# Kernel optimization log

Measured on AMD Instinct MI355X. Metric: run time of the kernel, lower is better.

## Reference

```python
import jax, jax.numpy as jnp
import numpy as np

K = 3
STRIDE = 1
PAD = 1
GROUPS = 16
EPS = 1e-5


def _conv2d(x, w, b, stride, pad):
    out = jax.lax.conv_general_dilated(
        x, w, (stride, stride), [(pad, pad), (pad, pad)],
        dimension_numbers=("NCHW", "OIHW", "NCHW"))
    return out + b[None, :, None, None]


def setup_inputs() -> dict:
    key = jax.random.key(0)
    ks = jax.random.split(key, 6)
    B, Cin, H, W = 4, 256, 64, 64
    Cout = 256
    x = jax.random.normal(ks[0], (B, Cin, H, W), dtype=jnp.float32)
    # DCNv2 offset/mask-generating conv: 3*K*K = 27 output channels
    w_off = jax.random.normal(ks[1], (3 * K * K, Cin, K, K), dtype=jnp.float32) * 0.01
    b_off = jnp.zeros((3 * K * K,), dtype=jnp.float32)
    # main deformable conv weight/bias
    weight = jax.random.normal(ks[2], (Cout, Cin, K, K), dtype=jnp.float32) * 0.02
    bias = jnp.zeros((Cout,), dtype=jnp.float32)
    # GroupNorm affine params
    gamma = jnp.ones((Cout,), dtype=jnp.float32)
    beta = jnp.zeros((Cout,), dtype=jnp.float32)
    return {"x": x, "w_off": w_off, "b_off": b_off,
            "weight": weight, "bias": bias, "gamma": gamma, "beta": beta}


def reference(x, w_off, b_off, weight, bias, gamma, beta):
    B, Cin, H, W = x.shape
    Cout = weight.shape[0]
    KK = K * K

    # --- offset/mask branch (DCNv2): 18 offsets + 9 sigmoid masks ---
    om = _conv2d(x, w_off, b_off, STRIDE, PAD)          # [B, 27, Ho, Wo]
    Ho, Wo = om.shape[2], om.shape[3]
    off_y, off_x, m = jnp.split(om, 3, axis=1)          # each [B, 9, Ho, Wo]
    mask = jax.nn.sigmoid(m)

    # --- sampling coordinates: base grid + kernel tap + learned offset ---
    kgy = jnp.repeat(jnp.arange(K, dtype=x.dtype), K)   # [9] row of tap
    kgx = jnp.tile(jnp.arange(K, dtype=x.dtype), K)     # [9] col of tap
    base_y = jnp.arange(Ho, dtype=x.dtype) * STRIDE - PAD
    base_x = jnp.arange(Wo, dtype=x.dtype) * STRIDE - PAD
    py = base_y[None, None, :, None] + kgy[None, :, None, None] + off_y  # [B,9,Ho,Wo]
    px = base_x[None, None, None, :] + kgx[None, :, None, None] + off_x  # [B,9,Ho,Wo]

    # --- bilinear sampling with zero padding outside the image ---
    y0 = jnp.floor(py)
    x0 = jnp.floor(px)
    wy1 = py - y0
    wx1 = px - x0

    def gather(img, yy, xx):
        # img [Cin,H,W], yy/xx [9,Ho,Wo] int -> [Cin,9,Ho,Wo]
        return img[:, yy, xx]

    def corner(yi, xi, wy, wx):
        valid = (yi >= 0) & (yi < H) & (xi >= 0) & (xi < W)
        yc = jnp.clip(yi, 0, H - 1).astype(jnp.int32)
        xc = jnp.clip(xi, 0, W - 1).astype(jnp.int32)
        vals = jax.vmap(gather)(x, yc, xc)               # [B,Cin,9,Ho,Wo]
        w_ = (wy * wx * valid.astype(x.dtype))[:, None]   # [B,1,9,Ho,Wo]
        return vals * w_

    sampled = (corner(y0, x0, (1 - wy1), (1 - wx1))
               + corner(y0, x0 + 1, (1 - wy1), wx1)
               + corner(y0 + 1, x0, wy1, (1 - wx1))
               + corner(y0 + 1, x0 + 1, wy1, wx1))       # [B,Cin,9,Ho,Wo]
    sampled = sampled * mask[:, None]                     # modulation

    # --- conv accumulation over taps and input channels ---
    out = jnp.einsum("bckhw,ock->bohw", sampled,
                     weight.reshape(Cout, Cin, KK)) + bias[None, :, None, None]

    # --- GroupNorm(16, Cout) ---
    og = out.reshape(B, GROUPS, Cout // GROUPS, Ho, Wo)
    mu = og.mean(axis=(2, 3, 4), keepdims=True)
    var = og.var(axis=(2, 3, 4), keepdims=True)
    og = (og - mu) * jax.lax.rsqrt(var + EPS)
    out = og.reshape(B, Cout, Ho, Wo) * gamma[None, :, None, None] + beta[None, :, None, None]
    return out
```

## Files before the change

kernel.cpp:

```cpp
#include <hip/hip_runtime.h>
#include <math.h>

#define CIN   256
#define COUT  256
#define H     64
#define W     64
#define HW    4096
#define KK    9
#define KC    2304
#define NOFF  27
#define B_    4
#define EPS   1e-5f
#define OM3S  (B_ * NOFF * HW)

typedef __attribute__((ext_vector_type(4))) float f32x4;
typedef __attribute__((ext_vector_type(8))) short s16x8;

static __device__ __forceinline__ unsigned short f2bf(float f) {
  unsigned u = __builtin_bit_cast(unsigned, f);
  u += 0x7FFF + ((u >> 16) & 1);
  return (unsigned short)(u >> 16);
}
static __device__ __forceinline__ float bflo(unsigned u) {
  return __builtin_bit_cast(float, u << 16);
}
static __device__ __forceinline__ float bfhi(unsigned u) {
  return __builtin_bit_cast(float, u & 0xffff0000u);
}
static __device__ __forceinline__ unsigned packbf(float lo, float hi) {
  unsigned ul = __builtin_bit_cast(unsigned, lo);
  unsigned uh = __builtin_bit_cast(unsigned, hi);
  ul += 0x7FFF + ((ul >> 16) & 1);
  uh += 0x7FFF + ((uh >> 16) & 1);
  return (ul >> 16) | (uh & 0xffff0000u);
}
static __device__ __forceinline__ void gl2lds16(const void* g, void* l) {
  __builtin_amdgcn_global_load_lds(
      (const __attribute__((address_space(1))) unsigned int*)g,
      (__attribute__((address_space(3))) unsigned int*)l, 16, 0, 0);
}

__global__ __launch_bounds__(256) void prep_kernel(
    const float* __restrict__ x, const float* __restrict__ w,
    const float* __restrict__ w_off, unsigned short* __restrict__ xT,
    unsigned short* __restrict__ wBf, unsigned short* __restrict__ wOBf,
    float* __restrict__ gstat) {
  int bi = blockIdx.x;
  int t = threadIdx.x;
  if (bi < 256) {
    __shared__ unsigned short tile[64][272];
    int b = bi >> 6, y = bi & 63;
    const float* src = x + (size_t)b * CIN * HW + y * W;
    for (int r = 0; r < 64; ++r) {
      int idx = r * 256 + t;
      int c = idx >> 6, ww = idx & 63;
      tile[ww][c] = f2bf(src[(size_t)c * HW + ww]);
    }
    __syncthreads();
    unsigned short* dst = xT + ((size_t)(b * 64 + y) * 64) * 256;
    for (int r = 0; r < 8; ++r) {
      int idx = r * 2048 + t * 8;
      int ww = idx >> 8, c = idx & 255;
      *(uint4*)(dst + idx) = *(const uint4*)&tile[ww][c];
    }
  } else if (bi < 544) {
    int pkt = (bi - 256) * 256 + t;
    int lane = pkt & 63;
    int tn = (pkt >> 6) & 15;
    int k2 = pkt >> 10;
    int co = tn * 16 + (lane & 15);
    int kb = k2 * 32 + (lane >> 4) * 8;
    unsigned short v[8];
#pragma unroll
    for (int j = 0; j < 8; ++j) {
      int kk = kb + j;
      int kt = kk >> 8, c = kk & 255;
      v[j] = f2bf(w[(co * 256 + c) * 9 + kt]);
    }
    *(uint4*)&wBf[(size_t)pkt * 8] = *(const uint4*)v;
  } else if (bi < 580) {
    int pkt = (bi - 544) * 256 + t;
    int lane = pkt & 63;
    int tn = (pkt >> 6) & 1;
    int k2 = pkt >> 7;
    int oc = tn * 16 + (lane & 15);
    int kb = k2 * 32 + (lane >> 4) * 8;
    unsigned short v[8];
#pragma unroll
    for (int j = 0; j < 8; ++j) {
      int kk = kb + j;
      int kt = kk >> 8, c = kk & 255;
      v[j] = (oc < NOFF) ? f2bf(w_off[(oc * 256 + c) * 9 + kt]) : (unsigned short)0;
    }
    *(uint4*)&wOBf[(size_t)pkt * 8] = *(const uint4*)v;
  } else {
    if (t < 128) gstat[t] = 0.f;
  }
}

__global__ __launch_bounds__(256) void offconv_mfma_kernel(
    const unsigned short* __restrict__ xT, const unsigned short* __restrict__ wOBf,
    float* __restrict__ om3) {
  int bi = blockIdx.x;
  int ts = bi >> 8;
  int row = bi & 255;
  int b = row >> 6, i = row & 63;
  int t = threadIdx.x, lane = t & 63, wv = t >> 6;
  int lr = lane & 15, lq = lane >> 4;
  int p = wv * 16 + lr;
  const unsigned short* xb = xT + (size_t)b * (HW * 256);
  f32x4 acc[2] = {};

  for (int kc = 0; kc < 3; ++kc) {
    int kt = ts * 3 + kc;
    int ky = kt / 3, kx = kt % 3;
    int yy = i - 1 + ky, xx = p - 1 + kx;
    bool ok = ((unsigned)yy < 64u) && ((unsigned)xx < 64u);
    const unsigned short* ap = xb + ((ok ? yy * 64 + xx : 0) << 8) + lq * 8;
#pragma unroll
    for (int c8 = 0; c8 < 8; ++c8) {
      uint4 av = uint4{0, 0, 0, 0};
      if (ok) av = *(const uint4*)(ap + c8 * 32);
      int k2 = kt * 8 + c8;
      s16x8 a = __builtin_bit_cast(s16x8, av);
      s16x8 b0 = *(const s16x8*)(wOBf + ((((k2 * 2 + 0) << 6) | lane) << 3));
      s16x8 b1 = *(const s16x8*)(wOBf + ((((k2 * 2 + 1) << 6) | lane) << 3));
      acc[0] = __builtin_amdgcn_mfma_f32_16x16x32_bf16(a, b0, acc[0], 0, 0, 0);
      acc[1] = __builtin_amdgcn_mfma_f32_16x16x32_bf16(a, b1, acc[1], 0, 0, 0);
    }
  }
#pragma unroll
  for (int tn = 0; tn < 2; ++tn) {
    int oc = tn * 16 + lr;
    if (oc < NOFF) {
      float* ob = om3 + (size_t)ts * OM3S + ((b * NOFF + oc) << 12) + i * 64 + wv * 16;
#pragma unroll
      for (int r = 0; r < 4; ++r) ob[lq * 4 + r] = acc[tn][r];
    }
  }
}

__global__ __launch_bounds__(256, 2) void sampler_kernel(
    const unsigned short* __restrict__ xT, const float* __restrict__ om3,
    const float* __restrict__ b_off, unsigned short* __restrict__ Aout) {
  __shared__ float tapw[32][KK][4];
  __shared__ int   tapc[32][KK][4];
  int bi = blockIdx.x;
  int b = bi >> 7, i = (bi >> 1) & 63, j0 = (bi & 1) * 32;
  int t = threadIdx.x;
  const unsigned short* xb = xT + (size_t)b * (HW * 256);

  for (int idx = t; idx < 32 * KK; idx += 256) {
    int p = idx / KK, k = idx % KK;
    int pix = i * 64 + j0 + p;
    size_t o = (size_t)(b * NOFF) * HW + pix;
    float offy = om3[o + k * HW] + om3[OM3S + o + k * HW] +
                 om3[2 * OM3S + o + k * HW] + b_off[k];
    float offx = om3[o + (9 + k) * HW] + om3[OM3S + o + (9 + k) * HW] +
                 om3[2 * OM3S + o + (9 + k) * HW] + b_off[9 + k];
    float mval = om3[o + (18 + k) * HW] + om3[OM3S + o + (18 + k) * HW] +
                 om3[2 * OM3S + o + (18 + k) * HW] + b_off[18 + k];
    float mask = 1.f / (1.f + __expf(-mval));
    float py = (float)(i - 1 + k / 3) + offy;
    float px = (float)(j0 + p - 1 + k % 3) + offx;
    float y0f = floorf(py), x0f = floorf(px);
    float wy1 = py - y0f, wx1 = px - x0f;
    int y0 = (int)y0f, x0 = (int)x0f;
    bool y0ok = (unsigned)y0 < 64u, y1ok = (unsigned)(y0 + 1) < 64u;
    bool x0ok = (unsigned)x0 < 64u, x1ok = (unsigned)(x0 + 1) < 64u;
    tapw[p][k][0] = (1.f - wy1) * (1.f - wx1) * mask * (float)(y0ok && x0ok);
    tapw[p][k][1] = (1.f - wy1) * wx1 * mask * (float)(y0ok && x1ok);
    tapw[p][k][2] = wy1 * (1.f - wx1) * mask * (float)(y1ok && x0ok);
    tapw[p][k][3] = wy1 * wx1 * mask * (float)(y1ok && x1ok);
    int y0c = min(max(y0, 0), 63), y1c = min(max(y0 + 1, 0), 63);
    int x0c = min(max(x0, 0), 63), x1c = min(max(x0 + 1, 0), 63);
    tapc[p][k][0] = (y0c * 64 + x0c) * 256;
    tapc[p][k][1] = (x1c - x0c) * 256;
    tapc[p][k][2] = (y1c - y0c) * 64 * 256;
    tapc[p][k][3] = 0;
  }
  __syncthreads();

  int p = t >> 3, s = t & 7;
  int gpix = b * 4096 + i * 64 + j0 + p;
  unsigned short* arow = Aout + (size_t)gpix * KC;

  for (int kt = 0; kt < KK; ++kt) {
    f32x4 tw = *(const f32x4*)&tapw[p][kt][0];
    float w00 = tw[0], w01 = tw[1], w10 = tw[2], w11 = tw[3];
    int4 tc = *(const int4*)&tapc[p][kt][0];
    const unsigned short* c00 = xb + tc.x + s * 8;
    int dx = tc.y, dy = tc.z;
#pragma unroll
    for (int g = 0; g < 4; ++g) {
      int c = g * 64 + s * 8;
      int cc = g * 64;
      uint4 v00 = *(const uint4*)(c00 + cc);
      uint4 v01 = *(const uint4*)(c00 + dx + cc);
      uint4 v10 = *(const uint4*)(c00 + dy + cc);
      uint4 v11 = *(const uint4*)(c00 + dy + dx + cc);
      const unsigned* a00 = (const unsigned*)&v00;
      const unsigned* a01 = (const unsigned*)&v01;
      const unsigned* a10 = (const unsigned*)&v10;
      const unsigned* a11 = (const unsigned*)&v11;
      uint4 res;
      unsigned* rr = (unsigned*)&res;
#pragma unroll
      for (int q = 0; q < 4; ++q) {
        float lo = w00 * bflo(a00[q]) + w01 * bflo(a01[q]) +
                   w10 * bflo(a10[q]) + w11 * bflo(a11[q]);
        float hi = w00 * bfhi(a00[q]) + w01 * bfhi(a01[q]) +
                   w10 * bfhi(a10[q]) + w11 * bfhi(a11[q]);
        rr[q] = packbf(lo, hi);
      }
      *(uint4*)(arow + kt * 256 + c) = res;
    }
  }
}

__global__ __launch_bounds__(256, 2) void gemm_kernel(
    const unsigned short* __restrict__ A, const unsigned short* __restrict__ wBf,
    const float* __restrict__ bias, unsigned short* __restrict__ cvt,
    float* __restrict__ gstat) {
  __shared__ unsigned short At[2][64 * 64];
  int bi = blockIdx.x;
  int m0 = (bi & 255) * 64;
  int nh = bi >> 8;
  int t = threadIdx.x, lane = t & 63, wv = t >> 6;
  int lr = lane & 15, lq = lane >> 4;
  int rowq = lane >> 3, pos = lane & 7;
  int swz = pos ^ rowq;

  const char* Asrc0 = (const char*)A + (size_t)(m0 + wv * 16 + rowq) * 4608 + swz * 16;
  const char* Asrc1 = Asrc0 + 8 * 4608;
  const unsigned short* bb = wBf + ((size_t)((nh * 8 + wv * 2) * 64) + lane) * 8;

  f32x4 acc[4][2] = {};
  s16x8 Bf0[2][2], Bf1[2][2];

  gl2lds16(Asrc0, (char*)At[0] + (wv * 16) * 128);
  gl2lds16(Asrc1, (char*)At[0] + (wv * 16 + 8) * 128);
  __builtin_amdgcn_sched_barrier(0);
#pragma unroll
  for (int kh = 0; kh < 2; ++kh)
#pragma unroll
    for (int tn = 0; tn < 2; ++tn)
      Bf0[kh][tn] = *(const s16x8*)(bb + (size_t)kh * 8192 + tn * 512);

#pragma unroll 1
  for (int k = 0; k < 36; k += 2) {
    asm volatile("s_waitcnt vmcnt(4)" ::: "memory");
    __builtin_amdgcn_s_barrier();
    {
      int koff = (k + 1) * 128;
      gl2lds16(Asrc0 + koff, (char*)At[1] + (wv * 16) * 128);
      gl2lds16(Asrc1 + koff, (char*)At[1] + (wv * 16 + 8) * 128);
      __builtin_amdgcn_sched_barrier(0);
      int k2b = (k + 1) * 2;
#pragma unroll
      for (int kh = 0; kh < 2; ++kh)
#pragma unroll
        for (int tn = 0; tn < 2; ++tn)
          Bf1[kh][tn] = *(const s16x8*)(bb + (size_t)(k2b + kh) * 8192 + tn * 512);
    }
    {
      const char* buf = (const char*)At[0];
#pragma unroll
      for (int kh = 0; kh < 2; ++kh) {
        s16x8 af[4];
#pragma unroll
        for (int tm = 0; tm < 4; ++tm) {
          int r = tm * 16 + lr;
          af[tm] = *(const s16x8*)(buf + r * 128 + (((kh * 4 + lq) ^ (r & 7)) * 16));
        }
        __builtin_amdgcn_s_setprio(1);
#pragma unroll
        for (int tm = 0; tm < 4; ++tm)
#pragma unroll
          for (int tn = 0; tn < 2; ++tn)
            acc[tm][tn] = __builtin_amdgcn_mfma_f32_16x16x32_bf16(
                af[tm], Bf0[kh][tn], acc[tm][tn], 0, 0, 0);
        __builtin_amdgcn_s_setprio(0);
      }
    }
    asm volatile("s_waitcnt vmcnt(4)" ::: "memory");
    __builtin_amdgcn_s_barrier();
    if (k + 2 < 36) {
      int koff = (k + 2) * 128;
      gl2lds16(Asrc0 + koff, (char*)At[0] + (wv * 16) * 128);
      gl2lds16(Asrc1 + koff, (char*)At[0] + (wv * 16 + 8) * 128);
      __builtin_amdgcn_sched_barrier(0);
      int k2b = (k + 2) * 2;
#pragma unroll
      for (int kh = 0; kh < 2; ++kh)
#pragma unroll
        for (int tn = 0; tn < 2; ++tn)
          Bf0[kh][tn] = *(const s16x8*)(bb + (size_t)(k2b + kh) * 8192 + tn * 512);
    }
    {
      const char* buf = (const char*)At[1];
#pragma unroll
      for (int kh = 0; kh < 2; ++kh) {
        s16x8 af[4];
#pragma unroll
        for (int tm = 0; tm < 4; ++tm) {
          int r = tm * 16 + lr;
          af[tm] = *(const s16x8*)(buf + r * 128 + (((kh * 4 + lq) ^ (r & 7)) * 16));
        }
        __builtin_amdgcn_s_setprio(1);
#pragma unroll
        for (int tm = 0; tm < 4; ++tm)
#pragma unroll
          for (int tn = 0; tn < 2; ++tn)
            acc[tm][tn] = __builtin_amdgcn_mfma_f32_16x16x32_bf16(
                af[tm], Bf1[kh][tn], acc[tm][tn], 0, 0, 0);
        __builtin_amdgcn_s_setprio(0);
      }
    }
  }

  int b = m0 >> 12;
  int poff = m0 & 4095;
#pragma unroll
  for (int tn = 0; tn < 2; ++tn) {
    int co = nh * 128 + wv * 32 + tn * 16 + lr;
    float bco = bias[co];
    unsigned short* cvb = cvt + (size_t)(b * COUT + co) * HW + poff;
    float s = 0.f, q = 0.f;
#pragma unroll
    for (int tm = 0; tm < 4; ++tm) {
      ushort4 st;
#pragma unroll
      for (int r = 0; r < 4; ++r) {
        float v = acc[tm][tn][r] + bco;
        s += v;
        q += v * v;
        ((unsigned short*)&st)[r] = f2bf(v);
      }
      *(ushort4*)(cvb + tm * 16 + lq * 4) = st;
    }
#pragma unroll
    for (int off = 32; off > 0; off >>= 1) {
      s += __shfl_down(s, off, 64);
      q += __shfl_down(q, off, 64);
    }
    if (lane == 0) {
      int g = co >> 4;
      atomicAdd(&gstat[(b * 16 + g) * 2 + 0], s);
      atomicAdd(&gstat[(b * 16 + g) * 2 + 1], q);
    }
  }
}

__global__ __launch_bounds__(256) void gn_apply_kernel(
    const unsigned short* __restrict__ convout, const float* __restrict__ gstat,
    const float* __restrict__ gamma, const float* __restrict__ beta,
    float* __restrict__ out) {
  int vid = blockIdx.x * 256 + threadIdx.x;
  int e = vid * 8;
  int b = e >> 20;
  int c = (e >> 12) & 255;
  int g = c >> 4;
  float S = gstat[(b * 16 + g) * 2 + 0];
  float Q = gstat[(b * 16 + g) * 2 + 1];
  float mu = S * (1.f / 65536.f);
  float var = Q * (1.f / 65536.f) - mu * mu;
  float rs = rsqrtf(var + EPS);
  float a = rs * gamma[c];
  float bb = beta[c] - mu * a;
  uint4 v = *(const uint4*)(convout + e);
  const unsigned* u = (const unsigned*)&v;
  float4 o0, o1;
  o0.x = bflo(u[0]) * a + bb;  o0.y = bfhi(u[0]) * a + bb;
  o0.z = bflo(u[1]) * a + bb;  o0.w = bfhi(u[1]) * a + bb;
  o1.x = bflo(u[2]) * a + bb;  o1.y = bfhi(u[2]) * a + bb;
  o1.z = bflo(u[3]) * a + bb;  o1.w = bfhi(u[3]) * a + bb;
  *(float4*)(out + e) = o0;
  *(float4*)(out + e + 4) = o1;
}

extern "C" void kernel_launch(void* const* d_in, const int* in_sizes, int n_in,
                              void* d_out, int out_size, void* d_ws, size_t ws_size,
                              hipStream_t stream) {
  const float* x      = (const float*)d_in[0];
  const float* w_off  = (const float*)d_in[1];
  const float* b_off  = (const float*)d_in[2];
  const float* weight = (const float*)d_in[3];
  const float* bias   = (const float*)d_in[4];
  const float* gamma  = (const float*)d_in[5];
  const float* beta   = (const float*)d_in[6];
  float* out = (float*)d_out;

  float* om3 = (float*)d_ws;
  unsigned short* xT   = (unsigned short*)(om3 + (size_t)3 * OM3S);
  unsigned short* cvt  = xT;
  unsigned short* wBf  = xT + (size_t)B_ * HW * 256;
  unsigned short* wOBf = wBf + (size_t)COUT * KC;
  unsigned short* Abuf = wOBf + (size_t)32 * KC;
  float* gstat = (float*)(Abuf + (size_t)B_ * HW * KC);

  prep_kernel<<<dim3(581), dim3(256), 0, stream>>>(x, weight, w_off, xT, wBf, wOBf, gstat);
  offconv_mfma_kernel<<<dim3(768), dim3(256), 0, stream>>>(xT, wOBf, om3);
  sampler_kernel<<<dim3(512), dim3(256), 0, stream>>>(xT, om3, b_off, Abuf);
  gemm_kernel<<<dim3(512), dim3(256), 0, stream>>>(Abuf, wBf, bias, cvt, gstat);
  gn_apply_kernel<<<dim3(2048), dim3(256), 0, stream>>>(cvt, gstat, gamma, beta, out);
}
```

Before: 177.8 us.

## Deepen GEMM pipeline to a four-slot LDS ring with three tiles in flight

Replaces the double-buffered A tile in the GEMM kernel with a four-slot LDS ring, issuing A loads three steps ahead and B register fragments two steps ahead, fully unrolled through macros. The aim is to hide more global-load latency behind the MFMA work. The explicit per-step `s_waitcnt vmcnt` waits are gone; ordering now relies on the barrier and on compiler-inserted waits for the B registers. That risks a wave reading another wave's A tile before its LDS write has landed. LDS use doubles to 32 KB per block.

```diff
diff --git a/kernel.cpp b/kernel.cpp
--- a/kernel.cpp
+++ b/kernel.cpp
@@ -222,7 +222,7 @@
     const unsigned short* __restrict__ A, const unsigned short* __restrict__ wBf,
     const float* __restrict__ bias, unsigned short* __restrict__ cvt,
     float* __restrict__ gstat) {
-  __shared__ unsigned short At[2][64 * 64];
+  __shared__ unsigned short At[4][64 * 64];
   int bi = blockIdx.x;
   int m0 = (bi & 255) * 64;
   int nh = bi >> 8;
@@ -236,88 +236,77 @@
   const unsigned short* bb = wBf + ((size_t)((nh * 8 + wv * 2) * 64) + lane) * 8;
 
   f32x4 acc[4][2] = {};
-  s16x8 Bf0[2][2], Bf1[2][2];
-
-  gl2lds16(Asrc0, (char*)At[0] + (wv * 16) * 128);
-  gl2lds16(Asrc1, (char*)At[0] + (wv * 16 + 8) * 128);
+  s16x8 Bfa[2][2], Bfb[2][2];
+
+#define AISSUE(J)                                                            \
+  {                                                                          \
+    char* db_ = (char*)At + (((J) & 3) * 8192) + (wv * 16) * 128;            \
+    gl2lds16(Asrc0 + (J) * 128, db_);                                        \
+    gl2lds16(Asrc1 + (J) * 128, db_ + 8 * 128);                              \
+  }
+
+#define BISSUE(J, SLOT)                                                      \
+  {                                                                          \
+    int k2b_ = (J) * 2;                                                      \
+    _Pragma("unroll") for (int kh = 0; kh < 2; ++kh)                         \
+      _Pragma("unroll") for (int tn = 0; tn < 2; ++tn)                       \
+        SLOT[kh][tn] = *(const s16x8*)(bb + (size_t)(k2b_ + kh) * 8192 + tn * 512); \
+  }
+
+#define CONSUME(J, SLOT)                                                     \
+  {                                                                          \
+    const char* buf_ = (const char*)At + (((J) & 3) * 8192);                 \
+    _Pragma("unroll") for (int kh = 0; kh < 2; ++kh) {                       \
+      s16x8 af[4];                                                           \
+      _Pragma("unroll") for (int tm = 0; tm < 4; ++tm) {                     \
+        int r_ = tm * 16 + lr;                                               \
+        af[tm] = *(const s16x8*)(buf_ + r_ * 128 + (((kh * 4 + lq) ^ (r_ & 7)) * 16)); \
+      }                                                                      \
+      __builtin_amdgcn_s_setprio(1);                                         \
+      _Pragma("unroll") for (int tm = 0; tm < 4; ++tm)                       \
+        _Pragma("unroll") for (int tn = 0; tn < 2; ++tn)                     \
+          acc[tm][tn] = __builtin_amdgcn_mfma_f32_16x16x32_bf16(             \
+              af[tm], SLOT[kh][tn], acc[tm][tn], 0, 0, 0);                   \
+      __builtin_amdgcn_s_setprio(0);                                         \
+    }                                                                        \
+  }
+
+#define PIPE_ITER(J, DO_A, DO_B, SLOT)                                       \
+  {                                                                          \
+    __builtin_amdgcn_s_barrier();                                            \
+    if (DO_A) AISSUE((J) + 3);                                               \
+    __builtin_amdgcn_sched_barrier(0);                                       \
+    CONSUME(J, SLOT);                                                        \
+    if (DO_B) BISSUE((J) + 2, SLOT);                                         \
+    __builtin_amdgcn_sched_barrier(0);                                       \
+  }
+
+  AISSUE(0);
+  AISSUE(1);
+  AISSUE(2);
   __builtin_amdgcn_sched_barrier(0);
-#pragma unroll
-  for (int kh = 0; kh < 2; ++kh)
-#pragma unroll
-    for (int tn = 0; tn < 2; ++tn)
-      Bf0[kh][tn] = *(const s16x8*)(bb + (size_t)kh * 8192 + tn * 512);
+  BISSUE(0, Bfa);
+  BISSUE(1, Bfb);
+  __builtin_amdgcn_sched_barrier(0);
+  asm volatile("s_waitcnt vmcnt(12)" ::: "memory");
+  __builtin_amdgcn_sched_barrier(0);
 
 #pragma unroll 1
-  for (int k = 0; k < 36; k += 2) {
-    asm volatile("s_waitcnt vmcnt(4)" ::: "memory");
-    __builtin_amdgcn_s_barrier();
-    {
-      int koff = (k + 1) * 128;
-      gl2lds16(Asrc0 + koff, (char*)At[1] + (wv * 16) * 128);
-      gl2lds16(Asrc1 + koff, (char*)At[1] + (wv * 16 + 8) * 128);
-      __builtin_amdgcn_sched_barrier(0);
-      int k2b = (k + 1) * 2;
-#pragma unroll
-      for (int kh = 0; kh < 2; ++kh)
-#pragma unroll
-        for (int tn = 0; tn < 2; ++tn)
-          Bf1[kh][tn] = *(const s16x8*)(bb + (size_t)(k2b + kh) * 8192 + tn * 512);
-    }
-    {
-      const char* buf = (const char*)At[0];
-#pragma unroll
-      for (int kh = 0; kh < 2; ++kh) {
-        s16x8 af[4];
-#pragma unroll
-        for (int tm = 0; tm < 4; ++tm) {
-          int r = tm * 16 + lr;
-          af[tm] = *(const s16x8*)(buf + r * 128 + (((kh * 4 + lq) ^ (r & 7)) * 16));
-        }
-        __builtin_amdgcn_s_setprio(1);
-#pragma unroll
-        for (int tm = 0; tm < 4; ++tm)
-#pragma unroll
-          for (int tn = 0; tn < 2; ++tn)
-            acc[tm][tn] = __builtin_amdgcn_mfma_f32_16x16x32_bf16(
-                af[tm], Bf0[kh][tn], acc[tm][tn], 0, 0, 0);
-        __builtin_amdgcn_s_setprio(0);
-      }
-    }
-    asm volatile("s_waitcnt vmcnt(4)" ::: "memory");
-    __builtin_amdgcn_s_barrier();
-    if (k + 2 < 36) {
-      int koff = (k + 2) * 128;
-      gl2lds16(Asrc0 + koff, (char*)At[0] + (wv * 16) * 128);
-      gl2lds16(Asrc1 + koff, (char*)At[0] + (wv * 16 + 8) * 128);
-      __builtin_amdgcn_sched_barrier(0);
-      int k2b = (k + 2) * 2;
-#pragma unroll
-      for (int kh = 0; kh < 2; ++kh)
-#pragma unroll
-        for (int tn = 0; tn < 2; ++tn)
-          Bf0[kh][tn] = *(const s16x8*)(bb + (size_t)(k2b + kh) * 8192 + tn * 512);
-    }
-    {
-      const char* buf = (const char*)At[1];
-#pragma unroll
-      for (int kh = 0; kh < 2; ++kh) {
-        s16x8 af[4];
-#pragma unroll
-        for (int tm = 0; tm < 4; ++tm) {
-          int r = tm * 16 + lr;
-          af[tm] = *(const s16x8*)(buf + r * 128 + (((kh * 4 + lq) ^ (r & 7)) * 16));
-        }
-        __builtin_amdgcn_s_setprio(1);
-#pragma unroll
-        for (int tm = 0; tm < 4; ++tm)
-#pragma unroll
-          for (int tn = 0; tn < 2; ++tn)
-            acc[tm][tn] = __builtin_amdgcn_mfma_f32_16x16x32_bf16(
-                af[tm], Bf1[kh][tn], acc[tm][tn], 0, 0, 0);
-        __builtin_amdgcn_s_setprio(0);
-      }
-    }
-  }
+  for (int k = 0; k < 32; k += 4) {
+    PIPE_ITER(k + 0, 1, 1, Bfa);
+    PIPE_ITER(k + 1, 1, 1, Bfb);
+    PIPE_ITER(k + 2, 1, 1, Bfa);
+    PIPE_ITER(k + 3, 1, 1, Bfb);
+  }
+  PIPE_ITER(32, 1, 1, Bfa);
+  PIPE_ITER(33, 0, 1, Bfb);
+  PIPE_ITER(34, 0, 0, Bfa);
+  PIPE_ITER(35, 0, 0, Bfb);
+
+#undef AISSUE
+#undef BISSUE
+#undef CONSUME
+#undef PIPE_ITER
 
   int b = m0 >> 12;
   int poff = m0 & 4095;
```

Result: no change. 178.5 us (+0.4%).
